# Kernel optimization log

Hardware: AMD Instinct MI355X
Metric: run time of the kernel (lower is better)

Reference implementation:

```python
import jax, jax.numpy as jnp
import numpy as np

INPUT_SIZE = 512
HIDDEN = 512
LAYERS = 4
T = 256
B = 64


def _weight_size():
    total = 0
    for l in range(LAYERS):
        insize = INPUT_SIZE if l == 0 else HIDDEN
        total += insize * 6 * HIDDEN + HIDDEN * 5 * HIDDEN
    return total


def setup_inputs() -> dict:
    key = jax.random.key(0)
    k1, k2, k3 = jax.random.split(key, 3)
    inputs = jax.random.normal(k1, (B, T, INPUT_SIZE), dtype=jnp.float32)
    lengths = jax.random.randint(k2, (B,), T // 2, T + 1)
    lengths = jnp.sort(lengths)[::-1].astype(jnp.int32)  # descending, like pack_padded
    weight = jax.random.normal(k3, (_weight_size(),), dtype=jnp.float32) * 0.05
    # bias: zeros except forget-gate block (second of 5) filled with 1, per layer
    b_layer = jnp.concatenate([
        jnp.zeros((HIDDEN,), jnp.float32),
        jnp.ones((HIDDEN,), jnp.float32),
        jnp.zeros((3 * HIDDEN,), jnp.float32),
    ])
    bias = jnp.tile(b_layer, LAYERS)
    return {"inputs": inputs, "weight": weight, "bias": bias, "lengths": lengths}


def _split_params(weight, bias):
    params = []
    idx = 0
    for l in range(LAYERS):
        insize = INPUT_SIZE if l == 0 else HIDDEN
        n = insize * 6 * HIDDEN
        W_ih = weight[idx:idx + n].reshape(insize, 6 * HIDDEN); idx += n
        n = HIDDEN * 5 * HIDDEN
        W_hh = weight[idx:idx + n].reshape(HIDDEN, 5 * HIDDEN); idx += n
        b = bias[l * 5 * HIDDEN:(l + 1) * 5 * HIDDEN]
        params.append((W_ih, W_hh, b))
    return params


def _reverse_padded(x, lengths):
    # x: [T, B, D]; reverse each sequence within its own length, keep padding in place
    t = jnp.arange(x.shape[0])[:, None]                      # [T, 1]
    L = lengths[None, :]                                     # [1, B]
    idx = jnp.where(t < L, L - 1 - t, t)                     # [T, B]
    return jnp.take_along_axis(x, idx[:, :, None], axis=0)


def _run_layer(x, W_ih, W_hh, b, mask):
    # x: [T, B, D], mask: [T, B, 1] (1.0 where t < length)
    H = HIDDEN
    xi = jnp.einsum('tbd,dg->tbg', x, W_ih)                  # [T, B, 6H] (batched GEMM)

    def step(carry, inp):
        h, c = carry
        xi_t, m = inp
        g = xi_t[:, :5 * H] + h @ W_hh + b                   # [B, 5H]
        i = jax.nn.sigmoid(g[:, 0 * H:1 * H])
        f = jax.nn.sigmoid(g[:, 1 * H:2 * H])
        gc = jnp.tanh(g[:, 2 * H:3 * H])
        o = jax.nn.sigmoid(g[:, 3 * H:4 * H])
        r = jax.nn.sigmoid(g[:, 4 * H:5 * H])                # highway transform gate
        lin = xi_t[:, 5 * H:]                                # highway linear projection of input
        c_new = (f * c + i * gc) * m
        h_new = (r * (o * jnp.tanh(c_new)) + (1.0 - r) * lin) * m
        return (h_new, c_new), h_new

    h0 = jnp.zeros((x.shape[1], H), x.dtype)
    (_, _), hs = jax.lax.scan(step, (h0, h0), (xi, mask))
    return hs                                                # [T, B, H]


def reference(inputs, weight, bias, lengths):
    x = jnp.transpose(inputs, (1, 0, 2))                     # [T, B, D]
    mask = (jnp.arange(T)[:, None] < lengths[None, :]).astype(x.dtype)[:, :, None]
    x = x * mask                                             # emulate packed-sequence zero padding
    for l, (W_ih, W_hh, b) in enumerate(_split_params(weight, bias)):
        rev = (l % 2 == 1)                                   # layers alternate direction
        if rev:
            x = _reverse_padded(x, lengths)
        h = _run_layer(x, W_ih, W_hh, b, mask)
        if rev:
            h = _reverse_padded(h, lengths)
        x = h
    return jnp.transpose(x, (1, 0, 2))                       # [B, T, H]
```

## Files before the change

kernel.cpp:

```cpp
#include <hip/hip_runtime.h>
#include <hip/hip_bf16.h>

#define T_STEPS 256
#define BATCH 64
#define HID 512
#define GATES 3072
#define NLAYERS 4
#define BT_GROUPS 4
#define GBLK 32
#define SCAN_THREADS 256
#define HSTR 520
#define GLP 84
#define POLL_VALVE 4096

typedef __bf16 bf16_t;
typedef _Float16 fp16_t;
typedef __attribute__((ext_vector_type(8))) __bf16 bf16x8;
typedef __attribute__((ext_vector_type(4))) float f32x4;
typedef __attribute__((ext_vector_type(4))) unsigned int u32x4;

__device__ __forceinline__ float sigm(float x){ return 1.0f/(1.0f + __expf(-x)); }
__device__ __forceinline__ float tanh_f(float x){ return 2.0f/(1.0f + __expf(-2.0f*x)) - 1.0f; }
__device__ __forceinline__ unsigned short f2bf(float x){ __bf16 b=(__bf16)x; return __builtin_bit_cast(unsigned short, b); }

__global__ void transpose_cast_kernel(const float* __restrict__ src, unsigned short* __restrict__ dst, int R, int C){
  __shared__ float tile[32][33];
  int tx = threadIdx.x & 31, ty = threadIdx.x >> 5;
  int c0 = blockIdx.x*32, r0 = blockIdx.y*32;
  #pragma unroll
  for(int i=0;i<4;i++){ int r = r0 + ty + i*8; tile[ty+i*8][tx] = src[(size_t)r*C + c0 + tx]; }
  __syncthreads();
  #pragma unroll
  for(int i=0;i<4;i++){ int c = c0 + ty + i*8; dst[(size_t)c*R + r0 + tx] = f2bf(tile[tx][ty+i*8]); }
}

__global__ void prep_x0_kernel(const float* __restrict__ inp, const int* __restrict__ lens, unsigned short* __restrict__ x0){
  int idx = blockIdx.x*blockDim.x + threadIdx.x;
  int e = idx*4;
  int d = e & (HID-1);
  int tb = e >> 9;
  int b = tb & (BATCH-1);
  int t = tb >> 6;
  const float4 v = *(const float4*)(inp + ((size_t)b*T_STEPS + t)*HID + d);
  float m = (t < lens[b]) ? 1.f : 0.f;
  ushort4 u; u.x=f2bf(v.x*m); u.y=f2bf(v.y*m); u.z=f2bf(v.z*m); u.w=f2bf(v.w*m);
  *(ushort4*)(x0 + ((size_t)t*BATCH + b)*HID + d) = u;
}

__global__ void __launch_bounds__(256,2)
xi_gemm_kernel(const unsigned short* __restrict__ A,
               const unsigned short* __restrict__ BT,
               fp16_t* __restrict__ C)
{
  __shared__ __align__(16) unsigned short As[128*72];
  __shared__ __align__(16) unsigned short Bs[128*72];
  const int tid = threadIdx.x, lane = tid & 63, wv = tid >> 6;
  const int frow = lane & 15, quad = lane >> 4;
  const int m0 = blockIdx.x*128, n0 = blockIdx.y*128;
  const int mh = (wv>>1)*64, nh = (wv&1)*64;
  const int sr = tid>>1, sk = (tid&1)*32;
  f32x4 acc[4][4];
  #pragma unroll
  for(int mt=0;mt<4;mt++)
    #pragma unroll
    for(int nt=0;nt<4;nt++) acc[mt][nt] = (f32x4){0.f,0.f,0.f,0.f};

  for(int kc=0;kc<512;kc+=64){
    #pragma unroll
    for(int i=0;i<4;i++){
      *(uint4*)(As + sr*72 + sk + i*8) = *(const uint4*)(A + (size_t)(m0+sr)*512 + kc + sk + i*8);
      *(uint4*)(Bs + sr*72 + sk + i*8) = *(const uint4*)(BT + (size_t)(n0+sr)*512 + kc + sk + i*8);
    }
    __syncthreads();
    #pragma unroll
    for(int ks=0;ks<2;ks++){
      bf16x8 av[4], bv[4];
      #pragma unroll
      for(int mt=0;mt<4;mt++) av[mt] = *(const bf16x8*)(As + (mh+mt*16+frow)*72 + ks*32 + quad*8);
      #pragma unroll
      for(int nt=0;nt<4;nt++) bv[nt] = *(const bf16x8*)(Bs + (nh+nt*16+frow)*72 + ks*32 + quad*8);
      #pragma unroll
      for(int mt=0;mt<4;mt++)
        #pragma unroll
        for(int nt=0;nt<4;nt++)
          acc[mt][nt] = __builtin_amdgcn_mfma_f32_16x16x32_bf16(av[mt], bv[nt], acc[mt][nt],0,0,0);
    }
    __syncthreads();
  }
  #pragma unroll
  for(int mt=0;mt<4;mt++)
    #pragma unroll
    for(int nt=0;nt<4;nt++)
      #pragma unroll
      for(int r4=0;r4<4;r4++)
        C[(size_t)(m0+mh+mt*16+quad*4+r4)*GATES + n0+nh+nt*16+frow] = (fp16_t)acc[mt][nt][r4];
}

__global__ void __launch_bounds__(SCAN_THREADS,1)
scan_kernel(const fp16_t* __restrict__ Xi,
            const unsigned short* __restrict__ WhhT,
            const float* __restrict__ bias_l,
            const int* __restrict__ lens,
            unsigned short* __restrict__ Hseq,
            unsigned short* __restrict__ xdst,
            float* __restrict__ dout,
            int rev)
{
  __shared__ __align__(16) unsigned short Al[16*HSTR];
  __shared__ float gl[64*GLP];
  __shared__ float bl[80];
  __shared__ int ll[16];

  const int tid = threadIdx.x;
  const int bt  = blockIdx.x & (BT_GROUPS-1);
  const int g   = blockIdx.x >> 2;
  const int lane = tid & 63, wv = tid >> 6;
  const int frow = lane & 15, quad = lane >> 4;

  for(int i=tid;i<80;i+=SCAN_THREADS) bl[i] = bias_l[(i>>4)*HID + g*16 + (i&15)];
  if(tid<16) ll[tid] = lens[bt*16+tid];
  __syncthreads();

  bf16x8 Bf[5][4];
  #pragma unroll
  for(int q=0;q<5;q++)
    #pragma unroll
    for(int j=0;j<4;j++)
      Bf[q][j] = *(const bf16x8*)(WhhT + (size_t)(q*HID + g*16 + frow)*HID + (wv + j*4)*32 + quad*8);

  const int cr = tid >> 4;
  const int jj = tid & 15;
  const int brow_g = bt*16 + cr;
  const int hcol   = g*16 + jj;
  const int L_r = ll[cr];
  float cst=0.f, hs=0.f;
  unsigned short hbf=0; int tprev=0;

  const size_t pofs[4] = {
    (size_t)((tid      )>>6)*HID + (size_t)((tid      )&63)*8,
    (size_t)((tid+256  )>>6)*HID + (size_t)((tid+256  )&63)*8,
    (size_t)((tid+512  )>>6)*HID + (size_t)((tid+512  )&63)*8,
    (size_t)((tid+768  )>>6)*HID + (size_t)((tid+768  )&63)*8 };

  for(int s=0; s<T_STEPS; s++){
    if(rev && s>0){
      if(dout) dout[((size_t)brow_g*T_STEPS + tprev)*HID + hcol] = hs;
      else     xdst[((size_t)tprev*BATCH + brow_g)*HID + hcol] = hbf;
    }

    bool valid = s < L_r;
    int tcur = rev ? (valid ? (L_r-1-s) : s) : s;
    const fp16_t* xr = Xi + ((size_t)tcur*BATCH + brow_g)*GATES + hcol;
    fp16_t x0v=xr[0], x1v=xr[512], x2v=xr[1024], x3v=xr[1536], x4v=xr[2048], x5v=xr[2560];

    u32x4 hv[4];
    if(s==0){
      #pragma unroll
      for(int i=0;i<4;i++) hv[i] = (u32x4){0u,0u,0u,0u};
    } else {
      const unsigned short* hb = Hseq + (size_t)(s-1)*BATCH*HID + (size_t)bt*16*HID;
      int it = 0;
      while(1){
        #pragma unroll
        for(int i=0;i<4;i++){
          const unsigned short* p = hb + pofs[i];
          asm volatile("global_load_dwordx4 %0, %1, off sc0 sc1" : "=v"(hv[i]) : "v"(p) : "memory");
        }
        asm volatile("s_waitcnt vmcnt(0)"
                     : "+v"(hv[0]), "+v"(hv[1]), "+v"(hv[2]), "+v"(hv[3])
                     :: "memory");
        __builtin_amdgcn_sched_barrier(0);
        unsigned int bad = 0u;
        #pragma unroll
        for(int i=0;i<4;i++){
          bad |= (unsigned)(hv[i][0] == 0xFFFFFFFFu);
          bad |= (unsigned)(hv[i][1] == 0xFFFFFFFFu);
          bad |= (unsigned)(hv[i][2] == 0xFFFFFFFFu);
          bad |= (unsigned)(hv[i][3] == 0xFFFFFFFFu);
        }
        if(!bad) break;
        if(++it > POLL_VALVE) break;
        __builtin_amdgcn_s_sleep(1);
      }
    }
    #pragma unroll
    for(int i=0;i<4;i++){
      int idx = tid + i*256;
      *(u32x4*)(Al + (idx>>6)*HSTR + (idx&63)*8) = hv[i];
    }
    __syncthreads();

    f32x4 acc[5];
    #pragma unroll
    for(int q=0;q<5;q++) acc[q] = (f32x4){0.f,0.f,0.f,0.f};
    #pragma unroll
    for(int j=0;j<4;j++){
      bf16x8 a = *(const bf16x8*)((const bf16_t*)Al + (size_t)frow*HSTR + (wv + j*4)*32 + quad*8);
      #pragma unroll
      for(int q=0;q<5;q++)
        acc[q] = __builtin_amdgcn_mfma_f32_16x16x32_bf16(a, Bf[q][j], acc[q],0,0,0);
    }
    #pragma unroll
    for(int q=0;q<5;q++)
      #pragma unroll
      for(int r4=0;r4<4;r4++)
        gl[(wv*16 + quad*4 + r4)*GLP + q*16 + frow] = acc[q][r4];
    __syncthreads();

    {
      float ga[5];
      #pragma unroll
      for(int q=0;q<5;q++){
        float sum = bl[q*16+jj];
        #pragma unroll
        for(int w=0;w<4;w++) sum += gl[(w*16+cr)*GLP + q*16 + jj];
        ga[q] = sum;
      }
      ga[0] += (float)x0v; ga[1] += (float)x1v; ga[2] += (float)x2v;
      ga[3] += (float)x3v; ga[4] += (float)x4v;
      float m = valid ? 1.f : 0.f;
      float gi=sigm(ga[0]), gf=sigm(ga[1]), gcv=tanh_f(ga[2]), go=sigm(ga[3]), grv=sigm(ga[4]);
      cst = (gf*cst + gi*gcv) * m;
      hs  = (grv*(go*tanh_f(cst)) + (1.f-grv)*(float)x5v) * m;
      hbf = f2bf(hs);
      tprev = tcur;

      int up = __shfl_down((int)(unsigned int)hbf, 1);
      if((jj&1)==0){
        unsigned int packed = (unsigned int)hbf | (((unsigned int)up & 0xFFFFu) << 16);
        unsigned int* dst = (unsigned int*)(Hseq + (size_t)s*BATCH*HID + (size_t)brow_g*HID + hcol);
        asm volatile("global_store_dword %0, %1, off sc0 sc1" :: "v"(dst), "v"(packed) : "memory");
      }
    }
  }

  if(rev){
    if(dout) dout[((size_t)brow_g*T_STEPS + tprev)*HID + hcol] = hs;
    else     xdst[((size_t)tprev*BATCH + brow_g)*HID + hcol] = hbf;
  }
}

extern "C" void kernel_launch(void* const* d_in, const int* in_sizes, int n_in,
                              void* d_out, int out_size, void* d_ws, size_t ws_size,
                              hipStream_t stream){
  const float* inp    = (const float*)d_in[0];
  const float* weight = (const float*)d_in[1];
  const float* bias   = (const float*)d_in[2];
  const int*   lens   = (const int*)d_in[3];
  float* dout = (float*)d_out;

  char* ws = (char*)d_ws;
  size_t off = 0;
  const size_t WTL = (size_t)(3072+2560)*512;
  unsigned short* WT = (unsigned short*)(ws+off); off += (size_t)NLAYERS*WTL*2;
  unsigned short* x0 = (unsigned short*)(ws+off); off += (size_t)T_STEPS*BATCH*HID*2;
  unsigned short* xA = (unsigned short*)(ws+off); off += (size_t)T_STEPS*BATCH*HID*2;
  fp16_t* Xi = (fp16_t*)(ws+off); off += (size_t)T_STEPS*BATCH*GATES*2;

  const size_t HSEQ_BYTES = (size_t)T_STEPS*BATCH*HID*2;

  const size_t WS_L = (size_t)512*3072 + (size_t)512*2560;
  for(int l=0;l<NLAYERS;l++){
    const float* wih = weight + l*WS_L;
    const float* whh = wih + (size_t)512*3072;
    unsigned short* wihT = WT + l*WTL;
    unsigned short* whhT = wihT + (size_t)3072*512;
    transpose_cast_kernel<<<dim3(3072/32,512/32),256,0,stream>>>(wih, wihT, 512, 3072);
    transpose_cast_kernel<<<dim3(2560/32,512/32),256,0,stream>>>(whh, whhT, 512, 2560);
  }
  prep_x0_kernel<<<8192,256,0,stream>>>(inp, lens, x0);

  const unsigned short* gemm_in[4] = {x0, xA, x0, xA};
  unsigned short*       hseq_l[4]  = {xA, xA, xA, x0};
  unsigned short*       xdst_l[4]  = {nullptr, x0, nullptr, nullptr};

  for(int l=0;l<NLAYERS;l++){
    xi_gemm_kernel<<<dim3(128,24),256,0,stream>>>(gemm_in[l], WT + l*WTL, Xi);
    hipMemsetAsync(hseq_l[l], 0xFF, HSEQ_BYTES, stream);
    scan_kernel<<<BT_GROUPS*GBLK, SCAN_THREADS, 0, stream>>>(
        Xi, WT + l*WTL + (size_t)3072*512,
        bias + (size_t)l*2560, lens, hseq_l[l],
        xdst_l[l], (l==3) ? dout : nullptr, l&1);
  }
}
```

Before: 3.063 ms.

## Load recurrent h fragments directly into MFMA registers and double-buffer gate LDS

Result: slower. 3.257 ms (+6.4%).

```diff
diff --git a/kernel.cpp b/kernel.cpp
--- a/kernel.cpp
+++ b/kernel.cpp
@@ -9,7 +9,6 @@
 #define BT_GROUPS 4
 #define GBLK 32
 #define SCAN_THREADS 256
-#define HSTR 520
 #define GLP 84
 #define POLL_VALVE 4096
 
@@ -106,8 +105,7 @@
             float* __restrict__ dout,
             int rev)
 {
-  __shared__ __align__(16) unsigned short Al[16*HSTR];
-  __shared__ float gl[64*GLP];
+  __shared__ float gl[2*64*GLP];
   __shared__ float bl[80];
   __shared__ int ll[16];
 
@@ -136,12 +134,6 @@
   float cst=0.f, hs=0.f;
   unsigned short hbf=0; int tprev=0;
 
-  const size_t pofs[4] = {
-    (size_t)((tid      )>>6)*HID + (size_t)((tid      )&63)*8,
-    (size_t)((tid+256  )>>6)*HID + (size_t)((tid+256  )&63)*8,
-    (size_t)((tid+512  )>>6)*HID + (size_t)((tid+512  )&63)*8,
-    (size_t)((tid+768  )>>6)*HID + (size_t)((tid+768  )&63)*8 };
-
   for(int s=0; s<T_STEPS; s++){
     if(rev && s>0){
       if(dout) dout[((size_t)brow_g*T_STEPS + tprev)*HID + hcol] = hs;
@@ -153,58 +145,54 @@
     const fp16_t* xr = Xi + ((size_t)tcur*BATCH + brow_g)*GATES + hcol;
     fp16_t x0v=xr[0], x1v=xr[512], x2v=xr[1024], x3v=xr[1536], x4v=xr[2048], x5v=xr[2560];
 
-    u32x4 hv[4];
+    u32x4 au[4];
     if(s==0){
       #pragma unroll
-      for(int i=0;i<4;i++) hv[i] = (u32x4){0u,0u,0u,0u};
+      for(int j=0;j<4;j++) au[j] = (u32x4){0u,0u,0u,0u};
     } else {
-      const unsigned short* hb = Hseq + (size_t)(s-1)*BATCH*HID + (size_t)bt*16*HID;
+      const unsigned short* hb = Hseq + (size_t)(s-1)*BATCH*HID
+                                      + (size_t)(bt*16 + frow)*HID + quad*8;
       int it = 0;
       while(1){
         #pragma unroll
-        for(int i=0;i<4;i++){
-          const unsigned short* p = hb + pofs[i];
-          asm volatile("global_load_dwordx4 %0, %1, off sc0 sc1" : "=v"(hv[i]) : "v"(p) : "memory");
+        for(int j=0;j<4;j++){
+          const unsigned short* p = hb + (wv + 4*j)*32;
+          asm volatile("global_load_dwordx4 %0, %1, off sc0 sc1" : "=v"(au[j]) : "v"(p) : "memory");
         }
         asm volatile("s_waitcnt vmcnt(0)"
-                     : "+v"(hv[0]), "+v"(hv[1]), "+v"(hv[2]), "+v"(hv[3])
+                     : "+v"(au[0]), "+v"(au[1]), "+v"(au[2]), "+v"(au[3])
                      :: "memory");
         __builtin_amdgcn_sched_barrier(0);
         unsigned int bad = 0u;
         #pragma unroll
-        for(int i=0;i<4;i++){
-          bad |= (unsigned)(hv[i][0] == 0xFFFFFFFFu);
-          bad |= (unsigned)(hv[i][1] == 0xFFFFFFFFu);
-          bad |= (unsigned)(hv[i][2] == 0xFFFFFFFFu);
-          bad |= (unsigned)(hv[i][3] == 0xFFFFFFFFu);
+        for(int j=0;j<4;j++){
+          bad |= (unsigned)(au[j][0] == 0xFFFFFFFFu);
+          bad |= (unsigned)(au[j][1] == 0xFFFFFFFFu);
+          bad |= (unsigned)(au[j][2] == 0xFFFFFFFFu);
+          bad |= (unsigned)(au[j][3] == 0xFFFFFFFFu);
         }
-        if(!bad) break;
+        if(!__any((int)bad)) break;
         if(++it > POLL_VALVE) break;
         __builtin_amdgcn_s_sleep(1);
       }
     }
-    #pragma unroll
-    for(int i=0;i<4;i++){
-      int idx = tid + i*256;
-      *(u32x4*)(Al + (idx>>6)*HSTR + (idx&63)*8) = hv[i];
-    }
-    __syncthreads();
 
     f32x4 acc[5];
     #pragma unroll
     for(int q=0;q<5;q++) acc[q] = (f32x4){0.f,0.f,0.f,0.f};
     #pragma unroll
     for(int j=0;j<4;j++){
-      bf16x8 a = *(const bf16x8*)((const bf16_t*)Al + (size_t)frow*HSTR + (wv + j*4)*32 + quad*8);
+      bf16x8 a = __builtin_bit_cast(bf16x8, au[j]);
       #pragma unroll
       for(int q=0;q<5;q++)
         acc[q] = __builtin_amdgcn_mfma_f32_16x16x32_bf16(a, Bf[q][j], acc[q],0,0,0);
     }
+    float* glp = gl + (s&1)*(64*GLP);
     #pragma unroll
     for(int q=0;q<5;q++)
       #pragma unroll
       for(int r4=0;r4<4;r4++)
-        gl[(wv*16 + quad*4 + r4)*GLP + q*16 + frow] = acc[q][r4];
+        glp[(wv*16 + quad*4 + r4)*GLP + q*16 + frow] = acc[q][r4];
     __syncthreads();
 
     {
@@ -213,7 +201,7 @@
       for(int q=0;q<5;q++){
         float sum = bl[q*16+jj];
         #pragma unroll
-        for(int w=0;w<4;w++) sum += gl[(w*16+cr)*GLP + q*16 + jj];
+        for(int w=0;w<4;w++) sum += glp[(w*16+cr)*GLP + q*16 + jj];
         ga[q] = sum;
       }
       ga[0] += (float)x0v; ga[1] += (float)x1v; ga[2] += (float)x2v;
```

## Halve scan grid by giving each block two 16-column hidden chunks

Applied to the files above, without the earlier changes.

Result: slower. 3.667 ms (+19.7%).

```diff
diff --git a/kernel.cpp b/kernel.cpp
--- a/kernel.cpp
+++ b/kernel.cpp
@@ -7,10 +7,10 @@
 #define GATES 3072
 #define NLAYERS 4
 #define BT_GROUPS 4
-#define GBLK 32
+#define GBLK 16
 #define SCAN_THREADS 256
 #define HSTR 520
-#define GLP 84
+#define GLP 164
 #define POLL_VALVE 4096
 
 typedef __bf16 bf16_t;
@@ -108,33 +108,36 @@
 {
   __shared__ __align__(16) unsigned short Al[16*HSTR];
   __shared__ float gl[64*GLP];
-  __shared__ float bl[80];
+  __shared__ float bl[160];
   __shared__ int ll[16];
 
   const int tid = threadIdx.x;
   const int bt  = blockIdx.x & (BT_GROUPS-1);
-  const int g   = blockIdx.x >> 2;
+  const int G   = blockIdx.x >> 2;
   const int lane = tid & 63, wv = tid >> 6;
   const int frow = lane & 15, quad = lane >> 4;
 
-  for(int i=tid;i<80;i+=SCAN_THREADS) bl[i] = bias_l[(i>>4)*HID + g*16 + (i&15)];
+  for(int i=tid;i<160;i+=SCAN_THREADS) bl[i] = bias_l[(i>>5)*HID + G*32 + (i&31)];
   if(tid<16) ll[tid] = lens[bt*16+tid];
   __syncthreads();
 
-  bf16x8 Bf[5][4];
-  #pragma unroll
-  for(int q=0;q<5;q++)
-    #pragma unroll
-    for(int j=0;j<4;j++)
-      Bf[q][j] = *(const bf16x8*)(WhhT + (size_t)(q*HID + g*16 + frow)*HID + (wv + j*4)*32 + quad*8);
+  bf16x8 Bf[2][5][4];
+  #pragma unroll
+  for(int c=0;c<2;c++)
+    #pragma unroll
+    for(int q=0;q<5;q++)
+      #pragma unroll
+      for(int j=0;j<4;j++)
+        Bf[c][q][j] = *(const bf16x8*)(WhhT + (size_t)(q*HID + G*32 + c*16 + frow)*HID + (wv + j*4)*32 + quad*8);
 
   const int cr = tid >> 4;
   const int jj = tid & 15;
   const int brow_g = bt*16 + cr;
-  const int hcol   = g*16 + jj;
+  const int hc0    = G*32 + jj;
+  const int hc1    = G*32 + 16 + jj;
   const int L_r = ll[cr];
-  float cst=0.f, hs=0.f;
-  unsigned short hbf=0; int tprev=0;
+  float cst[2] = {0.f,0.f}, hs[2] = {0.f,0.f};
+  unsigned short hbf[2] = {0,0}; int tprev=0;
 
   const size_t pofs[4] = {
     (size_t)((tid      )>>6)*HID + (size_t)((tid      )&63)*8,
@@ -144,14 +147,24 @@
 
   for(int s=0; s<T_STEPS; s++){
     if(rev && s>0){
-      if(dout) dout[((size_t)brow_g*T_STEPS + tprev)*HID + hcol] = hs;
-      else     xdst[((size_t)tprev*BATCH + brow_g)*HID + hcol] = hbf;
+      if(dout){
+        dout[((size_t)brow_g*T_STEPS + tprev)*HID + hc0] = hs[0];
+        dout[((size_t)brow_g*T_STEPS + tprev)*HID + hc1] = hs[1];
+      } else {
+        xdst[((size_t)tprev*BATCH + brow_g)*HID + hc0] = hbf[0];
+        xdst[((size_t)tprev*BATCH + brow_g)*HID + hc1] = hbf[1];
+      }
     }
 
     bool valid = s < L_r;
     int tcur = rev ? (valid ? (L_r-1-s) : s) : s;
-    const fp16_t* xr = Xi + ((size_t)tcur*BATCH + brow_g)*GATES + hcol;
-    fp16_t x0v=xr[0], x1v=xr[512], x2v=xr[1024], x3v=xr[1536], x4v=xr[2048], x5v=xr[2560];
+    const fp16_t* xr = Xi + ((size_t)tcur*BATCH + brow_g)*GATES + G*32 + jj;
+    fp16_t xv[2][6];
+    #pragma unroll
+    for(int c=0;c<2;c++)
+      #pragma unroll
+      for(int q=0;q<6;q++)
+        xv[c][q] = xr[c*16 + q*512];
 
     u32x4 hv[4];
     if(s==0){
@@ -190,53 +203,65 @@
     }
     __syncthreads();
 
-    f32x4 acc[5];
-    #pragma unroll
-    for(int q=0;q<5;q++) acc[q] = (f32x4){0.f,0.f,0.f,0.f};
+    f32x4 acc[2][5];
+    #pragma unroll
+    for(int c=0;c<2;c++)
+      #pragma unroll
+      for(int q=0;q<5;q++) acc[c][q] = (f32x4){0.f,0.f,0.f,0.f};
     #pragma unroll
     for(int j=0;j<4;j++){
       bf16x8 a = *(const bf16x8*)((const bf16_t*)Al + (size_t)frow*HSTR + (wv + j*4)*32 + quad*8);
       #pragma unroll
+      for(int c=0;c<2;c++)
+        #pragma unroll
+        for(int q=0;q<5;q++)
+          acc[c][q] = __builtin_amdgcn_mfma_f32_16x16x32_bf16(a, Bf[c][q][j], acc[c][q],0,0,0);
+    }
+    #pragma unroll
+    for(int c=0;c<2;c++)
+      #pragma unroll
       for(int q=0;q<5;q++)
-        acc[q] = __builtin_amdgcn_mfma_f32_16x16x32_bf16(a, Bf[q][j], acc[q],0,0,0);
-    }
-    #pragma unroll
-    for(int q=0;q<5;q++)
-      #pragma unroll
-      for(int r4=0;r4<4;r4++)
-        gl[(wv*16 + quad*4 + r4)*GLP + q*16 + frow] = acc[q][r4];
+        #pragma unroll
+        for(int r4=0;r4<4;r4++)
+          gl[(wv*16 + quad*4 + r4)*GLP + (c*5+q)*16 + frow] = acc[c][q][r4];
     __syncthreads();
 
     {
-      float ga[5];
-      #pragma unroll
-      for(int q=0;q<5;q++){
-        float sum = bl[q*16+jj];
-        #pragma unroll
-        for(int w=0;w<4;w++) sum += gl[(w*16+cr)*GLP + q*16 + jj];
-        ga[q] = sum;
+      float m = valid ? 1.f : 0.f;
+      tprev = tcur;
+      #pragma unroll
+      for(int c=0;c<2;c++){
+        float ga[5];
+        #pragma unroll
+        for(int q=0;q<5;q++){
+          float sum = bl[q*32 + c*16 + jj];
+          #pragma unroll
+          for(int w=0;w<4;w++) sum += gl[(w*16+cr)*GLP + (c*5+q)*16 + jj];
+          ga[q] = sum + (float)xv[c][q];
+        }
+        float gi=sigm(ga[0]), gf=sigm(ga[1]), gcv=tanh_f(ga[2]), go=sigm(ga[3]), grv=sigm(ga[4]);
+        cst[c] = (gf*cst[c] + gi*gcv) * m;
+        hs[c]  = (grv*(go*tanh_f(cst[c])) + (1.f-grv)*(float)xv[c][5]) * m;
+        hbf[c] = f2bf(hs[c]);
+
+        int up = __shfl_down((int)(unsigned int)hbf[c], 1);
+        if((jj&1)==0){
+          unsigned int packed = (unsigned int)hbf[c] | (((unsigned int)up & 0xFFFFu) << 16);
+          unsigned int* dst = (unsigned int*)(Hseq + (size_t)s*BATCH*HID + (size_t)brow_g*HID + G*32 + c*16 + jj);
+          asm volatile("global_store_dword %0, %1, off sc0 sc1" :: "v"(dst), "v"(packed) : "memory");
+        }
       }
-      ga[0] += (float)x0v; ga[1] += (float)x1v; ga[2] += (float)x2v;
-      ga[3] += (float)x3v; ga[4] += (float)x4v;
-      float m = valid ? 1.f : 0.f;
-      float gi=sigm(ga[0]), gf=sigm(ga[1]), gcv=tanh_f(ga[2]), go=sigm(ga[3]), grv=sigm(ga[4]);
-      cst = (gf*cst + gi*gcv) * m;
-      hs  = (grv*(go*tanh_f(cst)) + (1.f-grv)*(float)x5v) * m;
-      hbf = f2bf(hs);
-      tprev = tcur;
-
-      int up = __shfl_down((int)(unsigned int)hbf, 1);
-      if((jj&1)==0){
-        unsigned int packed = (unsigned int)hbf | (((unsigned int)up & 0xFFFFu) << 16);
-        unsigned int* dst = (unsigned int*)(Hseq + (size_t)s*BATCH*HID + (size_t)brow_g*HID + hcol);
-        asm volatile("global_store_dword %0, %1, off sc0 sc1" :: "v"(dst), "v"(packed) : "memory");
-      }
     }
   }
 
   if(rev){
-    if(dout) dout[((size_t)brow_g*T_STEPS + tprev)*HID + hcol] = hs;
-    else     xdst[((size_t)tprev*BATCH + brow_g)*HID + hcol] = hbf;
+    if(dout){
+      dout[((size_t)brow_g*T_STEPS + tprev)*HID + hc0] = hs[0];
+      dout[((size_t)brow_g*T_STEPS + tprev)*HID + hc1] = hs[1];
+    } else {
+      xdst[((size_t)tprev*BATCH + brow_g)*HID + hc0] = hbf[0];
+      xdst[((size_t)tprev*BATCH + brow_g)*HID + hc1] = hbf[1];
+    }
   }
 }
 
```
